# Performance work log

Hardware: AMD Instinct MI355X
Metric: run time of the kernel (lower is better)

## Reference

```python
import jax, jax.numpy as jnp
import numpy as np

B, H, W, C, HEADS = 8, 64, 64, 128, 4
H_SP, W_SP = 64, 8            # idx=0: H_sp = H, W_sp = split_size
HD = C // HEADS               # 32
N = H_SP * W_SP               # 512 tokens per window
SCALE = HD ** -0.5


def setup_inputs() -> dict:
    key = jax.random.key(0)
    k1, k2, k3 = jax.random.split(key, 3)
    return {
        "qkv": jax.random.normal(k1, (3, B, H * W, C), dtype=jnp.float32),
        "conv_w": jax.random.normal(k2, (C, 1, 3, 3), dtype=jnp.float32) * 0.1,
        "conv_b": jax.random.normal(k3, (C,), dtype=jnp.float32) * 0.1,
    }


def _to_windows(x):
    # x: [B, L, C] -> window tokens [Bw, N, C] with Bw = B * (H//H_SP) * (W//W_SP)
    x = x.reshape(B, H // H_SP, H_SP, W // W_SP, W_SP, C)
    x = x.transpose(0, 1, 3, 2, 4, 5).reshape(-1, N, C)
    return x


def _heads(x):
    # [Bw, N, C] -> [Bw, heads, N, hd]
    return x.reshape(-1, N, HEADS, HD).transpose(0, 2, 1, 3)


def reference(qkv, conv_w, conv_b):
    q, k, v = qkv[0], qkv[1], qkv[2]

    qw = _heads(_to_windows(q)) * SCALE   # [Bw, h, N, hd]
    kw = _heads(_to_windows(k))

    vwin = _to_windows(v)                 # [Bw, N, C]
    # LePE: depthwise 3x3 conv on each window (NHWC, feature_group_count=C)
    vimg = vwin.reshape(-1, H_SP, W_SP, C)
    w_hwio = conv_w.transpose(2, 3, 1, 0)  # [3,3,1,C]
    lepe = jax.lax.conv_general_dilated(
        vimg, w_hwio, window_strides=(1, 1), padding='SAME',
        dimension_numbers=('NHWC', 'HWIO', 'NHWC'), feature_group_count=C,
    ) + conv_b
    lepe = _heads(lepe.reshape(-1, N, C))  # [Bw, h, N, hd]
    vw = _heads(vwin)

    attn = jax.nn.softmax(jnp.einsum('whqd,whkd->whqk', qw, kw), axis=-1)
    out = jnp.einsum('whqk,whkd->whqd', attn, vw) + lepe  # [Bw, h, N, hd]

    # merge heads and windows back to [B, L, C]
    out = out.transpose(0, 2, 1, 3).reshape(-1, N, C)
    out = out.reshape(B, H // H_SP, W // W_SP, H_SP, W_SP, C)
    out = out.transpose(0, 1, 3, 2, 4, 5).reshape(B, H * W, C)
    return out
```

## Files before the change

kernel.cpp:

```cpp
#include <hip/hip_runtime.h>


namespace {
constexpr int Bn   = 8;
constexpr int Ww   = 64;
constexpr int Cc   = 128;
constexpr int HD   = 32;
constexpr int WSP  = 8;
constexpr int NTOK = 512;
constexpr int LL   = 64 * 64;
constexpr float SCALE = 0.17677669529663687f;
}

typedef __bf16 bf16x8 __attribute__((ext_vector_type(8)));
typedef float  f32x4  __attribute__((ext_vector_type(4)));
typedef unsigned int uint32x4 __attribute__((ext_vector_type(4)));

__device__ inline unsigned int pack2bf(float x, float y) {
    unsigned int ux = __builtin_bit_cast(unsigned int, x);
    unsigned int uy = __builtin_bit_cast(unsigned int, y);
    return ((ux + 0x8000u) >> 16) | ((uy + 0x8000u) & 0xFFFF0000u);
}
__device__ inline short bf1(float x) {
    unsigned int ux = __builtin_bit_cast(unsigned int, x);
    return (short)((ux + 0x8000u) >> 16);
}

__global__ __launch_bounds__(512, 1) void attn_kernel(const float* __restrict__ qkv,
                                                      const float* __restrict__ cw,
                                                      const float* __restrict__ cb,
                                                      float* __restrict__ out) {
    const int blk = blockIdx.x;
    const int w   = blk >> 2;
    const int h   = blk & 3;
    const int b   = w >> 3;
    const int wb  = w & 7;
    const int tid  = threadIdx.x;
    const int wid  = tid >> 6;
    const int lane = tid & 63;
    const int lq16 = lane & 15;
    const int lg   = lane >> 4;

    const float* qp = qkv;
    const float* kp = qkv + (size_t)Bn * LL * Cc;
    const float* vp = qkv + (size_t)2 * Bn * LL * Cc;

    __shared__ short K_lds[NTOK][40];
    __shared__ short VT_lds[HD][520];
    __shared__ short P_lds[8][64][72];

    bf16x8 qfrag[4];
#pragma unroll
    for (int qs = 0; qs < 4; ++qs) {
        const int tok = wid * 64 + qs * 16 + lq16;
        const int lqi = (tok >> 3) * Ww + wb * WSP + (tok & 7);
        const float* p = qp + ((size_t)b * LL + lqi) * Cc + h * HD + lg * 8;
        float4 a = *reinterpret_cast<const float4*>(p);
        float4 c = *reinterpret_cast<const float4*>(p + 4);
        uint32x4 u;
        u.x = pack2bf(a.x * SCALE, a.y * SCALE);
        u.y = pack2bf(a.z * SCALE, a.w * SCALE);
        u.z = pack2bf(c.x * SCALE, c.y * SCALE);
        u.w = pack2bf(c.z * SCALE, c.w * SCALE);
        qfrag[qs] = __builtin_bit_cast(bf16x8, u);
    }

    for (int i = tid; i < NTOK * 8; i += 512) {
        const int tok = i >> 3, d4 = i & 7;
        const int lqi = (tok >> 3) * Ww + wb * WSP + (tok & 7);
        const size_t base = ((size_t)b * LL + lqi) * Cc + h * HD + d4 * 4;
        float4 kv = *reinterpret_cast<const float4*>(kp + base);
        uint2 pk;
        pk.x = pack2bf(kv.x, kv.y);
        pk.y = pack2bf(kv.z, kv.w);
        *reinterpret_cast<uint2*>(&K_lds[tok][d4 * 4]) = pk;
        float4 vv = *reinterpret_cast<const float4*>(vp + base);
        VT_lds[d4 * 4 + 0][tok] = bf1(vv.x);
        VT_lds[d4 * 4 + 1][tok] = bf1(vv.y);
        VT_lds[d4 * 4 + 2][tok] = bf1(vv.z);
        VT_lds[d4 * 4 + 3][tok] = bf1(vv.w);
    }
    __syncthreads();

    f32x4 acc[4][2];
#pragma unroll
    for (int qs = 0; qs < 4; ++qs)
#pragma unroll
        for (int ds = 0; ds < 2; ++ds) acc[qs][ds] = (f32x4)(0.f);
    float lsum[4] = {0.f, 0.f, 0.f, 0.f};

    const f32x4 zero4 = (f32x4)(0.f);

    for (int kt = 0; kt < NTOK / 64; ++kt) {
        bf16x8 kfrag[4];
#pragma unroll
        for (int ks = 0; ks < 4; ++ks) {
            const int krow = kt * 64 + ks * 16 + lq16;
            kfrag[ks] = __builtin_bit_cast(bf16x8,
                *reinterpret_cast<const uint32x4*>(&K_lds[krow][lg * 8]));
        }
#pragma unroll
        for (int ks = 0; ks < 4; ++ks) {
#pragma unroll
            for (int qs = 0; qs < 4; ++qs) {
                f32x4 s = __builtin_amdgcn_mfma_f32_16x16x32_bf16(
                    kfrag[ks], qfrag[qs], zero4, 0, 0, 0);
                float e0 = __expf(s.x);
                float e1 = __expf(s.y);
                float e2 = __expf(s.z);
                float e3 = __expf(s.w);
                lsum[qs] += (e0 + e1) + (e2 + e3);
                uint2 pk;
                pk.x = pack2bf(e0, e1);
                pk.y = pack2bf(e2, e3);
                *reinterpret_cast<uint2*>(&P_lds[wid][qs * 16 + lq16][ks * 16 + lg * 4]) = pk;
            }
        }
#pragma unroll
        for (int at = 0; at < 2; ++at) {
            bf16x8 vfrag[2];
#pragma unroll
            for (int ds = 0; ds < 2; ++ds)
                vfrag[ds] = __builtin_bit_cast(bf16x8,
                    *reinterpret_cast<const uint32x4*>(
                        &VT_lds[ds * 16 + lq16][kt * 64 + at * 32 + lg * 8]));
#pragma unroll
            for (int qs = 0; qs < 4; ++qs) {
                bf16x8 pfrag = __builtin_bit_cast(bf16x8,
                    *reinterpret_cast<const uint32x4*>(
                        &P_lds[wid][qs * 16 + lq16][at * 32 + lg * 8]));
#pragma unroll
                for (int ds = 0; ds < 2; ++ds)
                    acc[qs][ds] = __builtin_amdgcn_mfma_f32_16x16x32_bf16(
                        pfrag, vfrag[ds], acc[qs][ds], 0, 0, 0);
            }
        }
    }

    float inv[4];
#pragma unroll
    for (int qs = 0; qs < 4; ++qs) {
        float s = lsum[qs];
        s += __shfl_xor(s, 16);
        s += __shfl_xor(s, 32);
        inv[qs] = 1.f / s;
    }

#pragma unroll
    for (int qs = 0; qs < 4; ++qs) {
#pragma unroll
        for (int r = 0; r < 4; ++r) {
            const float iv = __shfl(inv[qs], lg * 4 + r);
            const int tok = wid * 64 + qs * 16 + lg * 4 + r;
            const int lqi = (tok >> 3) * Ww + wb * WSP + (tok & 7);
            float* orow = out + ((size_t)b * LL + lqi) * Cc + h * HD;
#pragma unroll
            for (int ds = 0; ds < 2; ++ds)
                orow[ds * 16 + lq16] = acc[qs][ds][r] * iv;
        }
    }

    __syncthreads();

    const int d    = tid & 31;
    const int tg   = tid >> 5;
    const int tok0 = tg * 32;
    const int ch   = h * HD + d;

    float wreg[9];
#pragma unroll
    for (int wi = 0; wi < 9; ++wi) wreg[wi] = cw[ch * 9 + wi];
    const float bias = cb[ch];

    float vseg[48];
#pragma unroll
    for (int c = 0; c < 6; ++c) {
        int t = tok0 - 8 + c * 8;
        t = t < 0 ? 0 : (t > NTOK - 8 ? NTOK - 8 : t);
        const uint4 raw = *reinterpret_cast<const uint4*>(&VT_lds[d][t]);
        const unsigned u[4] = {raw.x, raw.y, raw.z, raw.w};
#pragma unroll
        for (int k = 0; k < 4; ++k) {
            vseg[c * 8 + k * 2 + 0] = __builtin_bit_cast(float, u[k] << 16);
            vseg[c * 8 + k * 2 + 1] = __builtin_bit_cast(float, u[k] & 0xFFFF0000u);
        }
    }

#pragma unroll
    for (int j = 0; j < 32; ++j) {
        const int tok = tok0 + j;
        const int wc  = j & 7;
        float a = bias;
#pragma unroll
        for (int dy = -1; dy <= 1; ++dy) {
            const int trow = tok + dy * 8;
            if (trow >= 0 && trow < NTOK) {
#pragma unroll
                for (int dx = -1; dx <= 1; ++dx) {
                    if (wc + dx < 0 || wc + dx > WSP - 1) continue;
                    a += wreg[(dy + 1) * 3 + (dx + 1)] * vseg[j + 8 + dy * 8 + dx];
                }
            }
        }
        const int lqi = (tok >> 3) * Ww + wb * WSP + (tok & 7);
        float* po = out + ((size_t)b * LL + lqi) * Cc + ch;
        *po += a;
    }
}

extern "C" void kernel_launch(void* const* d_in, const int* in_sizes, int n_in,
                              void* d_out, int out_size, void* d_ws, size_t ws_size,
                              hipStream_t stream) {
    const float* qkv = (const float*)d_in[0];
    const float* cw  = (const float*)d_in[1];
    const float* cb  = (const float*)d_in[2];
    float* out = (float*)d_out;

    attn_kernel<<<256, 512, 0, stream>>>(qkv, cw, cb, out);
}
```

Before: 35.62 us.

## Switch to 32x32 MFMA with register-resident P and fused LePE epilogue

Replaces the 16x16x32 MFMA tiling with 32x32x16 tiles. The softmax probabilities stay in registers, with v_permlane32_swap reshuffling them into the A-operand layout, so the P round-trip through LDS goes away. The query rows are split across two blocks, doubling the grid to 512 and allowing higher occupancy through launch bounds, and the exponent scale is folded into Q so exp2 can be used. The LePE conv is fused into the output write, removing the read-modify-write of out and the second barrier. In exchange, each block redundantly stages the full K/V for its window, which doubles global loads of K and V.

```diff
diff --git a/kernel.cpp b/kernel.cpp
--- a/kernel.cpp
+++ b/kernel.cpp
@@ -9,11 +9,13 @@
 constexpr int WSP  = 8;
 constexpr int NTOK = 512;
 constexpr int LL   = 64 * 64;
-constexpr float SCALE = 0.17677669529663687f;
+constexpr float SCALE_L2E = 0.17677669529663687f * 1.4426950408889634f;
+constexpr int KPAD = 36;
+constexpr int VPAD = 524;
 }
 
 typedef __bf16 bf16x8 __attribute__((ext_vector_type(8)));
-typedef float  f32x4  __attribute__((ext_vector_type(4)));
+typedef float  f32x16 __attribute__((ext_vector_type(16)));
 typedef unsigned int uint32x4 __attribute__((ext_vector_type(4)));
 
 __device__ inline unsigned int pack2bf(float x, float y) {
@@ -26,185 +28,156 @@
     return (short)((ux + 0x8000u) >> 16);
 }
 
-__global__ __launch_bounds__(512, 1) void attn_kernel(const float* __restrict__ qkv,
+__global__ __launch_bounds__(512, 4) void attn_kernel(const float* __restrict__ qkv,
                                                       const float* __restrict__ cw,
                                                       const float* __restrict__ cb,
                                                       float* __restrict__ out) {
     const int blk = blockIdx.x;
-    const int w   = blk >> 2;
-    const int h   = blk & 3;
+    const int w   = blk >> 3;
+    const int h   = (blk >> 1) & 3;
+    const int qh  = blk & 1;
     const int b   = w >> 3;
     const int wb  = w & 7;
-    const int tid  = threadIdx.x;
-    const int wid  = tid >> 6;
+    const int tid = threadIdx.x;
+    const int wv  = tid >> 6;
     const int lane = tid & 63;
-    const int lq16 = lane & 15;
-    const int lg   = lane >> 4;
+    const int l31 = lane & 31;
+    const int h5  = lane >> 5;
 
     const float* qp = qkv;
     const float* kp = qkv + (size_t)Bn * LL * Cc;
     const float* vp = qkv + (size_t)2 * Bn * LL * Cc;
 
-    __shared__ short K_lds[NTOK][40];
-    __shared__ short VT_lds[HD][520];
-    __shared__ short P_lds[8][64][72];
+    __shared__ short K_lds[NTOK][KPAD];
+    __shared__ short VT_lds[HD][VPAD];
 
-    bf16x8 qfrag[4];
+    const int qtok = qh * 256 + wv * 32 + l31;
+    const int qlqi = (qtok >> 3) * Ww + wb * WSP + (qtok & 7);
+    bf16x8 qf[2];
+    {
+        const float* p = qp + ((size_t)b * LL + qlqi) * Cc + h * HD + h5 * 8;
 #pragma unroll
-    for (int qs = 0; qs < 4; ++qs) {
-        const int tok = wid * 64 + qs * 16 + lq16;
-        const int lqi = (tok >> 3) * Ww + wb * WSP + (tok & 7);
-        const float* p = qp + ((size_t)b * LL + lqi) * Cc + h * HD + lg * 8;
-        float4 a = *reinterpret_cast<const float4*>(p);
-        float4 c = *reinterpret_cast<const float4*>(p + 4);
-        uint32x4 u;
-        u.x = pack2bf(a.x * SCALE, a.y * SCALE);
-        u.y = pack2bf(a.z * SCALE, a.w * SCALE);
-        u.z = pack2bf(c.x * SCALE, c.y * SCALE);
-        u.w = pack2bf(c.z * SCALE, c.w * SCALE);
-        qfrag[qs] = __builtin_bit_cast(bf16x8, u);
+        for (int dc = 0; dc < 2; ++dc) {
+            float4 a = *reinterpret_cast<const float4*>(p + dc * 16);
+            float4 c = *reinterpret_cast<const float4*>(p + dc * 16 + 4);
+            uint32x4 u;
+            u.x = pack2bf(a.x * SCALE_L2E, a.y * SCALE_L2E);
+            u.y = pack2bf(a.z * SCALE_L2E, a.w * SCALE_L2E);
+            u.z = pack2bf(c.x * SCALE_L2E, c.y * SCALE_L2E);
+            u.w = pack2bf(c.z * SCALE_L2E, c.w * SCALE_L2E);
+            qf[dc] = __builtin_bit_cast(bf16x8, u);
+        }
     }
 
     for (int i = tid; i < NTOK * 8; i += 512) {
-        const int tok = i >> 3, d4 = i & 7;
+        const int tok = i >> 3, j = i & 7;
         const int lqi = (tok >> 3) * Ww + wb * WSP + (tok & 7);
-        const size_t base = ((size_t)b * LL + lqi) * Cc + h * HD + d4 * 4;
+        const size_t base = ((size_t)b * LL + lqi) * Cc + h * HD + j * 4;
         float4 kv = *reinterpret_cast<const float4*>(kp + base);
         uint2 pk;
         pk.x = pack2bf(kv.x, kv.y);
         pk.y = pack2bf(kv.z, kv.w);
-        *reinterpret_cast<uint2*>(&K_lds[tok][d4 * 4]) = pk;
+        *reinterpret_cast<uint2*>(&K_lds[tok][j * 4]) = pk;
         float4 vv = *reinterpret_cast<const float4*>(vp + base);
-        VT_lds[d4 * 4 + 0][tok] = bf1(vv.x);
-        VT_lds[d4 * 4 + 1][tok] = bf1(vv.y);
-        VT_lds[d4 * 4 + 2][tok] = bf1(vv.z);
-        VT_lds[d4 * 4 + 3][tok] = bf1(vv.w);
+        VT_lds[j * 4 + 0][tok] = bf1(vv.x);
+        VT_lds[j * 4 + 1][tok] = bf1(vv.y);
+        VT_lds[j * 4 + 2][tok] = bf1(vv.z);
+        VT_lds[j * 4 + 3][tok] = bf1(vv.w);
     }
     __syncthreads();
 
-    f32x4 acc[4][2];
+    f32x16 acc = (f32x16)(0.f);
+    float lsum = 0.f;
+    const f32x16 z16 = (f32x16)(0.f);
+
+    for (int kt = 0; kt < 16; ++kt) {
+        const int krow = kt * 32 + l31;
+        bf16x8 kf[2];
 #pragma unroll
-    for (int qs = 0; qs < 4; ++qs)
+        for (int dc = 0; dc < 2; ++dc) {
+            const uint2 a0 = *reinterpret_cast<const uint2*>(&K_lds[krow][dc * 16 + h5 * 8]);
+            const uint2 a1 = *reinterpret_cast<const uint2*>(&K_lds[krow][dc * 16 + h5 * 8 + 4]);
+            uint32x4 u; u.x = a0.x; u.y = a0.y; u.z = a1.x; u.w = a1.y;
+            kf[dc] = __builtin_bit_cast(bf16x8, u);
+        }
+        f32x16 s = z16;
+        s = __builtin_amdgcn_mfma_f32_32x32x16_bf16(kf[0], qf[0], s, 0, 0, 0);
+        s = __builtin_amdgcn_mfma_f32_32x32x16_bf16(kf[1], qf[1], s, 0, 0, 0);
+
+        float pe[16];
 #pragma unroll
-        for (int ds = 0; ds < 2; ++ds) acc[qs][ds] = (f32x4)(0.f);
-    float lsum[4] = {0.f, 0.f, 0.f, 0.f};
+        for (int i = 0; i < 16; ++i) pe[i] = exp2f(s[i]);
+        {
+            float t0 = 0.f, t1 = 0.f;
+#pragma unroll
+            for (int i = 0; i < 8; ++i) { t0 += pe[2 * i]; t1 += pe[2 * i + 1]; }
+            lsum += t0 + t1;
+        }
+        unsigned dw[8];
+#pragma unroll
+        for (int i = 0; i < 8; ++i) dw[i] = pack2bf(pe[2 * i], pe[2 * i + 1]);
 
-    const f32x4 zero4 = (f32x4)(0.f);
-
-    for (int kt = 0; kt < NTOK / 64; ++kt) {
-        bf16x8 kfrag[4];
 #pragma unroll
-        for (int ks = 0; ks < 4; ++ks) {
-            const int krow = kt * 64 + ks * 16 + lq16;
-            kfrag[ks] = __builtin_bit_cast(bf16x8,
-                *reinterpret_cast<const uint32x4*>(&K_lds[krow][lg * 8]));
-        }
-#pragma unroll
-        for (int ks = 0; ks < 4; ++ks) {
-#pragma unroll
-            for (int qs = 0; qs < 4; ++qs) {
-                f32x4 s = __builtin_amdgcn_mfma_f32_16x16x32_bf16(
-                    kfrag[ks], qfrag[qs], zero4, 0, 0, 0);
-                float e0 = __expf(s.x);
-                float e1 = __expf(s.y);
-                float e2 = __expf(s.z);
-                float e3 = __expf(s.w);
-                lsum[qs] += (e0 + e1) + (e2 + e3);
-                uint2 pk;
-                pk.x = pack2bf(e0, e1);
-                pk.y = pack2bf(e2, e3);
-                *reinterpret_cast<uint2*>(&P_lds[wid][qs * 16 + lq16][ks * 16 + lg * 4]) = pk;
-            }
-        }
-#pragma unroll
-        for (int at = 0; at < 2; ++at) {
-            bf16x8 vfrag[2];
-#pragma unroll
-            for (int ds = 0; ds < 2; ++ds)
-                vfrag[ds] = __builtin_bit_cast(bf16x8,
-                    *reinterpret_cast<const uint32x4*>(
-                        &VT_lds[ds * 16 + lq16][kt * 64 + at * 32 + lg * 8]));
-#pragma unroll
-            for (int qs = 0; qs < 4; ++qs) {
-                bf16x8 pfrag = __builtin_bit_cast(bf16x8,
-                    *reinterpret_cast<const uint32x4*>(
-                        &P_lds[wid][qs * 16 + lq16][at * 32 + lg * 8]));
-#pragma unroll
-                for (int ds = 0; ds < 2; ++ds)
-                    acc[qs][ds] = __builtin_amdgcn_mfma_f32_16x16x32_bf16(
-                        pfrag, vfrag[ds], acc[qs][ds], 0, 0, 0);
-            }
+        for (int kw = 0; kw < 2; ++kw) {
+            unsigned a0 = dw[4 * kw + 0], b0 = dw[4 * kw + 2];
+            unsigned a1 = dw[4 * kw + 1], b1 = dw[4 * kw + 3];
+            asm("v_permlane32_swap_b32 %0, %1" : "+v"(a0), "+v"(b0));
+            asm("v_permlane32_swap_b32 %0, %1" : "+v"(a1), "+v"(b1));
+            uint32x4 pu; pu.x = a0; pu.y = a1; pu.z = b0; pu.w = b1;
+            const int kcol = kt * 32 + kw * 16 + h5 * 8;
+            const uint2 v0 = *reinterpret_cast<const uint2*>(&VT_lds[l31][kcol]);
+            const uint2 v1 = *reinterpret_cast<const uint2*>(&VT_lds[l31][kcol + 4]);
+            uint32x4 vu; vu.x = v0.x; vu.y = v0.y; vu.z = v1.x; vu.w = v1.y;
+            acc = __builtin_amdgcn_mfma_f32_32x32x16_bf16(
+                __builtin_bit_cast(bf16x8, pu), __builtin_bit_cast(bf16x8, vu), acc, 0, 0, 0);
         }
     }
 
-    float inv[4];
-#pragma unroll
-    for (int qs = 0; qs < 4; ++qs) {
-        float s = lsum[qs];
-        s += __shfl_xor(s, 16);
-        s += __shfl_xor(s, 32);
-        inv[qs] = 1.f / s;
-    }
+    lsum += __shfl_xor(lsum, 32);
+    const float inv = 1.f / lsum;
 
-#pragma unroll
-    for (int qs = 0; qs < 4; ++qs) {
-#pragma unroll
-        for (int r = 0; r < 4; ++r) {
-            const float iv = __shfl(inv[qs], lg * 4 + r);
-            const int tok = wid * 64 + qs * 16 + lg * 4 + r;
-            const int lqi = (tok >> 3) * Ww + wb * WSP + (tok & 7);
-            float* orow = out + ((size_t)b * LL + lqi) * Cc + h * HD;
-#pragma unroll
-            for (int ds = 0; ds < 2; ++ds)
-                orow[ds * 16 + lq16] = acc[qs][ds][r] * iv;
-        }
-    }
-
-    __syncthreads();
-
-    const int d    = tid & 31;
-    const int tg   = tid >> 5;
-    const int tok0 = tg * 32;
-    const int ch   = h * HD + d;
-
+    const int ch = h * HD + l31;
     float wreg[9];
 #pragma unroll
     for (int wi = 0; wi < 9; ++wi) wreg[wi] = cw[ch * 9 + wi];
     const float bias = cb[ch];
 
-    float vseg[48];
+    const int tok0 = qh * 256 + wv * 32;
+    float vseg[52];
+    {
+        const int segbase = tok0 + 4 * h5 - 12;
 #pragma unroll
-    for (int c = 0; c < 6; ++c) {
-        int t = tok0 - 8 + c * 8;
-        t = t < 0 ? 0 : (t > NTOK - 8 ? NTOK - 8 : t);
-        const uint4 raw = *reinterpret_cast<const uint4*>(&VT_lds[d][t]);
-        const unsigned u[4] = {raw.x, raw.y, raw.z, raw.w};
-#pragma unroll
-        for (int k = 0; k < 4; ++k) {
-            vseg[c * 8 + k * 2 + 0] = __builtin_bit_cast(float, u[k] << 16);
-            vseg[c * 8 + k * 2 + 1] = __builtin_bit_cast(float, u[k] & 0xFFFF0000u);
+        for (int c2 = 0; c2 < 13; ++c2) {
+            int t = segbase + 4 * c2;
+            t = t < 0 ? 0 : (t > NTOK - 4 ? NTOK - 4 : t);
+            const uint2 u = *reinterpret_cast<const uint2*>(&VT_lds[l31][t]);
+            vseg[c2 * 4 + 0] = __builtin_bit_cast(float, u.x << 16);
+            vseg[c2 * 4 + 1] = __builtin_bit_cast(float, u.x & 0xFFFF0000u);
+            vseg[c2 * 4 + 2] = __builtin_bit_cast(float, u.y << 16);
+            vseg[c2 * 4 + 3] = __builtin_bit_cast(float, u.y & 0xFFFF0000u);
         }
     }
 
 #pragma unroll
-    for (int j = 0; j < 32; ++j) {
-        const int tok = tok0 + j;
-        const int wc  = j & 7;
-        float a = bias;
+    for (int r = 0; r < 16; ++r) {
+        const int c_r = (r & 3) + 8 * (r >> 2);
+        const float iv = __shfl(inv, c_r + 4 * h5);
+        const int tok = tok0 + c_r + 4 * h5;
+        float cv = bias;
 #pragma unroll
         for (int dy = -1; dy <= 1; ++dy) {
-            const int trow = tok + dy * 8;
-            if (trow >= 0 && trow < NTOK) {
+            const bool rowok = (unsigned)(tok + dy * 8) < (unsigned)NTOK;
 #pragma unroll
-                for (int dx = -1; dx <= 1; ++dx) {
-                    if (wc + dx < 0 || wc + dx > WSP - 1) continue;
-                    a += wreg[(dy + 1) * 3 + (dx + 1)] * vseg[j + 8 + dy * 8 + dx];
-                }
+            for (int dx = -1; dx <= 1; ++dx) {
+                const int idx = c_r + 12 + dy * 8 + dx;
+                bool ok = rowok;
+                if (dx == -1) ok = ok && (((r & 3) != 0) || (h5 != 0));
+                if (dx == +1) ok = ok && (((r & 3) != 3) || (h5 == 0));
+                cv += ok ? wreg[(dy + 1) * 3 + (dx + 1)] * vseg[idx] : 0.f;
             }
         }
         const int lqi = (tok >> 3) * Ww + wb * WSP + (tok & 7);
-        float* po = out + ((size_t)b * LL + lqi) * Cc + ch;
-        *po += a;
+        out[((size_t)b * LL + lqi) * Cc + ch] = acc[r] * iv + cv;
     }
 }
 
@@ -216,5 +189,5 @@
     const float* cb  = (const float*)d_in[2];
     float* out = (float*)d_out;
 
-    attn_kernel<<<256, 512, 0, stream>>>(qkv, cw, cb, out);
+    attn_kernel<<<512, 512, 0, stream>>>(qkv, cw, cb, out);
 }
```

Result: slower. 42.03 us (+18.0%).
